# Optimization experiments

Hardware: AMD Instinct MI355X
Metric: run time of the kernel (lower is better)

## Reference

```python
import jax, jax.numpy as jnp
import numpy as np

N = 25000; E = 100000; H = 64; NODE_IN = 32; EDGE_IN = 16; L = 3


def _lin(key, fan_in, fan_out):
    kw, kb = jax.random.split(key)
    s = 1.0 / np.sqrt(fan_in)
    W = jax.random.uniform(kw, (fan_out, fan_in), minval=-s, maxval=s, dtype=jnp.float32)
    b = jax.random.uniform(kb, (fan_out,), minval=-s, maxval=s, dtype=jnp.float32)
    return W, b


def setup_inputs() -> dict:
    key = jax.random.key(0)
    ks = jax.random.split(key, 16)
    x = jax.random.normal(ks[0], (N, NODE_IN), dtype=jnp.float32)
    edge_attr = jax.random.normal(ks[1], (E, EDGE_IN), dtype=jnp.float32)
    edge_index = jax.random.randint(ks[2], (2, E), 0, N, dtype=jnp.int32)
    Wn1, bn1 = _lin(ks[3], NODE_IN, H)
    Wn2, bn2 = _lin(ks[4], H, H)
    Wn3, bn3 = _lin(ks[5], H, H)
    We1, be1 = _lin(ks[6], EDGE_IN, H)
    We2, be2 = _lin(ks[7], H, H)
    We3, be3 = _lin(ks[8], H, H * H)
    roots = jax.random.normal(ks[9], (L, H, H), dtype=jnp.float32) / np.sqrt(H)
    conv_bias = jnp.zeros((L, H), dtype=jnp.float32)
    s = 1.0 / np.sqrt(H)
    gru_Wih = jax.random.uniform(ks[10], (3 * H, H), minval=-s, maxval=s, dtype=jnp.float32)
    gru_Whh = jax.random.uniform(ks[11], (3 * H, H), minval=-s, maxval=s, dtype=jnp.float32)
    gru_bih = jax.random.uniform(ks[12], (3 * H,), minval=-s, maxval=s, dtype=jnp.float32)
    gru_bhh = jax.random.uniform(ks[13], (3 * H,), minval=-s, maxval=s, dtype=jnp.float32)
    return dict(x=x, edge_attr=edge_attr,
                Wn1=Wn1, bn1=bn1, Wn2=Wn2, bn2=bn2, Wn3=Wn3, bn3=bn3,
                We1=We1, be1=be1, We2=We2, be2=be2, We3=We3, be3=be3,
                roots=roots, conv_bias=conv_bias,
                gru_Wih=gru_Wih, gru_Whh=gru_Whh, gru_bih=gru_bih, gru_bhh=gru_bhh,
                edge_index=edge_index)


def _mpnn_forward(x, edge_attr, Wn1, bn1, Wn2, bn2, Wn3, bn3,
                  We1, be1, We2, be2, We3, be3,
                  roots, conv_bias, gru_Wih, gru_Whh, gru_bih, gru_bhh, edge_index):
    src, dst = edge_index[0], edge_index[1]
    # mlp_in: Linear-ReLU-Linear-ReLU-Linear
    h = jax.nn.relu(x @ Wn1.T + bn1)
    h = jax.nn.relu(h @ Wn2.T + bn2)
    h = h @ Wn3.T + bn3  # [N, H]
    # edge MLP is shared across all NNConv layers and edge_attr is constant -> compute once
    ew = jax.nn.relu(edge_attr @ We1.T + be1)
    ew = jax.nn.relu(ew @ We2.T + be2)
    ew = (ew @ We3.T + be3).reshape(E, H, H)  # per-edge weight [E, in, out]
    hidden = jnp.zeros((x.shape[0], H), dtype=h.dtype)  # GRU hidden (1 layer)
    for l in range(L):
        # NNConv: message_e = h[src_e] @ W_e, scatter-add to dst, plus root term and bias
        msg = jnp.einsum('ei,eio->eo', h[src], ew)
        aggr = jax.ops.segment_sum(msg, dst, num_segments=N)
        m = aggr + h @ roots[l] + conv_bias[l]  # [N, H]
        # GRU step (seq_len=1, batch=N)
        gi = m @ gru_Wih.T + gru_bih
        gh = hidden @ gru_Whh.T + gru_bhh
        i_r, i_z, i_n = jnp.split(gi, 3, axis=-1)
        h_r, h_z, h_n = jnp.split(gh, 3, axis=-1)
        r = jax.nn.sigmoid(i_r + h_r)
        z = jax.nn.sigmoid(i_z + h_z)
        n = jnp.tanh(i_n + r * h_n)
        hidden = (1.0 - z) * n + z * hidden
        h = hidden  # output of 1-layer GRU == new hidden
    return h


def reference(x, edge_attr, Wn1, bn1, Wn2, bn2, Wn3, bn3,
              We1, be1, We2, be2, We3, be3,
              roots, conv_bias, gru_Wih, gru_Whh, gru_bih, gru_bhh, edge_index):
    return _mpnn_forward(x, edge_attr, Wn1, bn1, Wn2, bn2, Wn3, bn3,
                         We1, be1, We2, be2, We3, be3,
                         roots, conv_bias, gru_Wih, gru_Whh, gru_bih, gru_bhh, edge_index)
```

## Files before the change

kernel.cpp:

```cpp
#include <hip/hip_runtime.h>
#include <math.h>

#define NN 25000
#define NE 100000

typedef _Float16 f16;
typedef _Float16 half8 __attribute__((ext_vector_type(8)));
typedef float f32x4 __attribute__((ext_vector_type(4)));

__global__ __launch_bounds__(256) void prep_all(
    const float* __restrict__ Wn1, const float* __restrict__ Wn2,
    const float* __restrict__ Wn3, const float* __restrict__ We1,
    const float* __restrict__ We2, const float* __restrict__ Wih,
    const float* __restrict__ Whh, const float* __restrict__ We3,
    const float* __restrict__ be3, float* __restrict__ T,
    f16* __restrict__ Wf16)
{
    int f = blockIdx.x * 256 + threadIdx.x;
    if (f < 39936) {
        if (f < 2048)       { int j = f;         T[f] = Wn1[(j & 63) * 32 + (j >> 6)]; }
        else if (f < 6144)  { int j = f - 2048;  T[f] = Wn2[(j & 63) * 64 + (j >> 6)]; }
        else if (f < 10240) { int j = f - 6144;  T[f] = Wn3[(j & 63) * 64 + (j >> 6)]; }
        else if (f < 11264) { int j = f - 10240; T[f] = We1[(j & 63) * 16 + (j >> 6)]; }
        else if (f < 15360) { int j = f - 11264; T[f] = We2[(j & 63) * 64 + (j >> 6)]; }
        else if (f < 27648) { int j = f - 15360; T[f] = Wih[(j % 192) * 64 + (j / 192)]; }
        else                { int j = f - 27648; T[f] = Whh[(j % 192) * 64 + (j / 192)]; }
    } else {
        int g = f - 39936;
        if (g < 262144) Wf16[g] = (f16)We3[g];
        else {
            int j = g - 262144; int o = (j >> 6), k = j & 63;
            Wf16[g] = (f16)be3[k * 64 + o];
        }
    }
}

__global__ __launch_bounds__(256) void node_mlp(
    const float* __restrict__ x, const float* __restrict__ T,
    const float* __restrict__ bn1, const float* __restrict__ bn2,
    const float* __restrict__ bn3,
    float* __restrict__ hbuf, f16* __restrict__ h16, float* __restrict__ aggr)
{
    __shared__ float sx[4][8][32];
    __shared__ float sh1[4][8][64];
    const float* Wn1T = T;
    const float* Wn2T = T + 2048;
    const float* Wn3T = T + 6144;
    int w = threadIdx.x >> 6, lane = threadIdx.x & 63;
    int n0 = blockIdx.x * 32 + w * 8;
    if (n0 >= NN) return;
    #pragma unroll
    for (int jj = 0; jj < 4; ++jj) {
        int f = jj * 64 + lane;
        sx[w][f >> 5][f & 31] = x[(size_t)(n0 + (f >> 5)) * 32 + (f & 31)];
    }
    float a[8];
    #pragma unroll
    for (int j = 0; j < 8; ++j) a[j] = bn1[lane];
    for (int i = 0; i < 32; i += 4) {
        float4 bb[8];
        #pragma unroll
        for (int j = 0; j < 8; ++j) bb[j] = *(const float4*)&sx[w][j][i];
        #pragma unroll
        for (int ii = 0; ii < 4; ++ii) {
            float wv = Wn1T[(i + ii) * 64 + lane];
            #pragma unroll
            for (int j = 0; j < 8; ++j) a[j] += ((const float*)&bb[j])[ii] * wv;
        }
    }
    #pragma unroll
    for (int j = 0; j < 8; ++j) { sh1[w][j][lane] = fmaxf(a[j], 0.f); a[j] = bn2[lane]; }
    for (int i = 0; i < 64; i += 4) {
        float4 bb[8];
        #pragma unroll
        for (int j = 0; j < 8; ++j) bb[j] = *(const float4*)&sh1[w][j][i];
        #pragma unroll
        for (int ii = 0; ii < 4; ++ii) {
            float wv = Wn2T[(i + ii) * 64 + lane];
            #pragma unroll
            for (int j = 0; j < 8; ++j) a[j] += ((const float*)&bb[j])[ii] * wv;
        }
    }
    #pragma unroll
    for (int j = 0; j < 8; ++j) { sh1[w][j][lane] = fmaxf(a[j], 0.f); a[j] = bn3[lane]; }
    for (int i = 0; i < 64; i += 4) {
        float4 bb[8];
        #pragma unroll
        for (int j = 0; j < 8; ++j) bb[j] = *(const float4*)&sh1[w][j][i];
        #pragma unroll
        for (int ii = 0; ii < 4; ++ii) {
            float wv = Wn3T[(i + ii) * 64 + lane];
            #pragma unroll
            for (int j = 0; j < 8; ++j) a[j] += ((const float*)&bb[j])[ii] * wv;
        }
    }
    #pragma unroll
    for (int j = 0; j < 8; ++j) {
        size_t idx = (size_t)(n0 + j) * 64 + lane;
        hbuf[idx] = a[j];
        h16[idx]  = (f16)a[j];
        aggr[idx] = 0.f;
    }
}

__global__ __launch_bounds__(256) void edge_mlp(
    const float* __restrict__ ea, const float* __restrict__ T,
    const float* __restrict__ be1, const float* __restrict__ be2,
    f16* __restrict__ ew16)
{
    __shared__ float sa[4][8][16];
    __shared__ float st[4][8][64];
    const float* We1T = T + 10240;
    const float* We2T = T + 11264;
    int w = threadIdx.x >> 6, lane = threadIdx.x & 63;
    int e0 = blockIdx.x * 32 + w * 8;
    if (e0 >= NE) return;
    #pragma unroll
    for (int jj = 0; jj < 2; ++jj) {
        int f = jj * 64 + lane;
        sa[w][f >> 4][f & 15] = ea[(size_t)(e0 + (f >> 4)) * 16 + (f & 15)];
    }
    float a[8];
    #pragma unroll
    for (int j = 0; j < 8; ++j) a[j] = be1[lane];
    for (int i = 0; i < 16; i += 4) {
        float4 bb[8];
        #pragma unroll
        for (int j = 0; j < 8; ++j) bb[j] = *(const float4*)&sa[w][j][i];
        #pragma unroll
        for (int ii = 0; ii < 4; ++ii) {
            float wv = We1T[(i + ii) * 64 + lane];
            #pragma unroll
            for (int j = 0; j < 8; ++j) a[j] += ((const float*)&bb[j])[ii] * wv;
        }
    }
    #pragma unroll
    for (int j = 0; j < 8; ++j) { st[w][j][lane] = fmaxf(a[j], 0.f); a[j] = be2[lane]; }
    for (int i = 0; i < 64; i += 4) {
        float4 bb[8];
        #pragma unroll
        for (int j = 0; j < 8; ++j) bb[j] = *(const float4*)&st[w][j][i];
        #pragma unroll
        for (int ii = 0; ii < 4; ++ii) {
            float wv = We2T[(i + ii) * 64 + lane];
            #pragma unroll
            for (int j = 0; j < 8; ++j) a[j] += ((const float*)&bb[j])[ii] * wv;
        }
    }
    #pragma unroll
    for (int j = 0; j < 8; ++j)
        ew16[(size_t)(e0 + j) * 64 + lane] = (f16)fmaxf(a[j], 0.f);
}

__device__ __forceinline__ half8 splat8(f16 v)
{ half8 r = { v, v, v, v, v, v, v, v }; return r; }

__device__ __forceinline__ void mfma_block(
    const char* bb, int swzA, int swzB,
    half8 aA0, half8 aA1, half8 aB0, half8 aB1, f32x4 (&acc)[2][4])
{
    half8 b00 = *(const half8*)(bb + 0    + swzA);
    half8 b01 = *(const half8*)(bb + 0    + swzB);
    half8 b10 = *(const half8*)(bb + 2048 + swzA);
    half8 b11 = *(const half8*)(bb + 2048 + swzB);
    half8 b20 = *(const half8*)(bb + 4096 + swzA);
    half8 b21 = *(const half8*)(bb + 4096 + swzB);
    half8 b30 = *(const half8*)(bb + 6144 + swzA);
    half8 b31 = *(const half8*)(bb + 6144 + swzB);
    acc[0][0] = __builtin_amdgcn_mfma_f32_16x16x32_f16(aA0, b00, acc[0][0], 0, 0, 0);
    acc[0][0] = __builtin_amdgcn_mfma_f32_16x16x32_f16(aA1, b01, acc[0][0], 0, 0, 0);
    acc[0][1] = __builtin_amdgcn_mfma_f32_16x16x32_f16(aA0, b10, acc[0][1], 0, 0, 0);
    acc[0][1] = __builtin_amdgcn_mfma_f32_16x16x32_f16(aA1, b11, acc[0][1], 0, 0, 0);
    acc[0][2] = __builtin_amdgcn_mfma_f32_16x16x32_f16(aA0, b20, acc[0][2], 0, 0, 0);
    acc[0][2] = __builtin_amdgcn_mfma_f32_16x16x32_f16(aA1, b21, acc[0][2], 0, 0, 0);
    acc[0][3] = __builtin_amdgcn_mfma_f32_16x16x32_f16(aA0, b30, acc[0][3], 0, 0, 0);
    acc[0][3] = __builtin_amdgcn_mfma_f32_16x16x32_f16(aA1, b31, acc[0][3], 0, 0, 0);
    acc[1][0] = __builtin_amdgcn_mfma_f32_16x16x32_f16(aB0, b00, acc[1][0], 0, 0, 0);
    acc[1][0] = __builtin_amdgcn_mfma_f32_16x16x32_f16(aB1, b01, acc[1][0], 0, 0, 0);
    acc[1][1] = __builtin_amdgcn_mfma_f32_16x16x32_f16(aB0, b10, acc[1][1], 0, 0, 0);
    acc[1][1] = __builtin_amdgcn_mfma_f32_16x16x32_f16(aB1, b11, acc[1][1], 0, 0, 0);
    acc[1][2] = __builtin_amdgcn_mfma_f32_16x16x32_f16(aB0, b20, acc[1][2], 0, 0, 0);
    acc[1][2] = __builtin_amdgcn_mfma_f32_16x16x32_f16(aB1, b21, acc[1][2], 0, 0, 0);
    acc[1][3] = __builtin_amdgcn_mfma_f32_16x16x32_f16(aB0, b30, acc[1][3], 0, 0, 0);
    acc[1][3] = __builtin_amdgcn_mfma_f32_16x16x32_f16(aB1, b31, acc[1][3], 0, 0, 0);
}

__global__ __launch_bounds__(256) void msg_mfma(
    const f16* __restrict__ h16, const f16* __restrict__ ew16,
    const f16* __restrict__ Wf16, const int* __restrict__ edge_index,
    float* __restrict__ aggr)
{
    __shared__ f16 sh_h[128][72];
    __shared__ f16 sh_ring[4][4096];
    __shared__ int sh_dst[128];
    int t = threadIdx.x, lane = t & 63, wv = t >> 6;
    int e0 = blockIdx.x * 128;
    char* ringc = (char*)&sh_ring[0][0];

    const uint4* gW = (const uint4*)Wf16;
    uint4 r0 = gW[t], r1 = gW[256 + t], r2 = gW[512 + t], r3 = gW[768 + t];

    {
        int row = t >> 1, part = t & 1;
        int e = e0 + row;
        bool valid = e < NE;
        int ec = valid ? e : NE - 1;
        int src = edge_index[ec];
        const uint4* hp = (const uint4*)(h16 + (size_t)src * 64 + part * 32);
        const uint4* ep = (const uint4*)(ew16 + (size_t)ec * 64 + part * 32);
        uint4 z = make_uint4(0u, 0u, 0u, 0u);
        uint4 h0 = hp[0], h1 = hp[1], h2 = hp[2], h3 = hp[3];
        uint4 g0 = valid ? ep[0] : z;
        uint4 g1 = valid ? ep[1] : z;
        uint4 g2 = valid ? ep[2] : z;
        uint4 g3 = valid ? ep[3] : z;
        *(uint4*)&sh_h[row][part * 32]      = h0;
        *(uint4*)&sh_h[row][part * 32 + 8]  = h1;
        *(uint4*)&sh_h[row][part * 32 + 16] = h2;
        *(uint4*)&sh_h[row][part * 32 + 24] = h3;
        int rb = row * 128, key = (row & 7) << 4;
        *(uint4*)(ringc + rb + ((part * 64 +  0) ^ key)) = g0;
        *(uint4*)(ringc + rb + ((part * 64 + 16) ^ key)) = g1;
        *(uint4*)(ringc + rb + ((part * 64 + 32) ^ key)) = g2;
        *(uint4*)(ringc + rb + ((part * 64 + 48) ^ key)) = g3;
        if (lane < 32) {
            int e2 = e0 + wv * 32 + lane;
            sh_dst[wv * 32 + lane] = (e2 < NE) ? edge_index[NE + e2] : -1;
        }
    }

    int r16 = lane & 15, kq = lane >> 4;
    int row0 = wv * 32 + r16, row1 = row0 + 16;

    int k0 = (row0 & 7) << 4, k1 = (row1 & 7) << 4;
    half8 evA0 = *(const half8*)(ringc + row0 * 128 + ((kq * 16) ^ k0));
    half8 evA1 = *(const half8*)(ringc + row0 * 128 + ((64 + kq * 16) ^ k0));
    half8 evB0 = *(const half8*)(ringc + row1 * 128 + ((kq * 16) ^ k1));
    half8 evB1 = *(const half8*)(ringc + row1 * 128 + ((64 + kq * 16) ^ k1));

    __syncthreads();

    int d0 = t * 16, d1 = 4096 + t * 16;
    int dsw0 = d0 ^ (((d0 >> 7) & 7) << 4);
    int dsw1 = d1 ^ (((d1 >> 7) & 7) << 4);

    *(uint4*)(ringc + dsw0) = r0;
    *(uint4*)(ringc + dsw1) = r1;
    *(uint4*)(ringc + 8192 + dsw0) = r2;
    *(uint4*)(ringc + 8192 + dsw1) = r3;
    r0 = gW[2 * 512 + t]; r1 = gW[2 * 512 + 256 + t];
    r2 = gW[3 * 512 + t]; r3 = gW[3 * 512 + 256 + t];
    __syncthreads();

    f32x4 acc[2][4];
    #pragma unroll
    for (int m = 0; m < 2; ++m)
        #pragma unroll
        for (int n = 0; n < 4; ++n) acc[m][n] = (f32x4){0, 0, 0, 0};

    int swzA = (kq << 4) ^ ((r16 & 7) << 4);
    int swzB = ((kq << 4) | 64) ^ ((r16 & 7) << 4);

    for (int i8 = 0; i8 < 8; ++i8) {
        half8 hA = *(const half8*)&sh_h[row0][i8 * 8];
        half8 hB = *(const half8*)&sh_h[row1][i8 * 8];
        #pragma unroll
        for (int w2 = 0; w2 < 4; ++w2) {
            const char* pairR = ringc + (w2 & 1) * 16384 + r16 * 128;
            #pragma unroll
            for (int s = 0; s < 2; ++s) {
                f16 hsA = hA[w2 * 2 + s];
                f16 hsB = hB[w2 * 2 + s];
                mfma_block(pairR + s * 8192, swzA, swzB,
                           evA0 * splat8(hsA), evA1 * splat8(hsA),
                           evB0 * splat8(hsB), evB1 * splat8(hsB), acc);
            }
            char* wb = ringc + ((w2 + 1) & 1) * 16384;
            *(uint4*)(wb + dsw0) = r0;
            *(uint4*)(wb + dsw1) = r1;
            *(uint4*)(wb + 8192 + dsw0) = r2;
            *(uint4*)(wb + 8192 + dsw1) = r3;
            int jw = i8 * 4 + w2;
            int sA = jw * 2 + 4; if (sA > 64) sA = 64;
            int sB = jw * 2 + 5; if (sB > 64) sB = 64;
            r0 = gW[(size_t)sA * 512 + t]; r1 = gW[(size_t)sA * 512 + 256 + t];
            r2 = gW[(size_t)sB * 512 + t]; r3 = gW[(size_t)sB * 512 + 256 + t];
            __syncthreads();
        }
    }

    {
        const char* bb = ringc + r16 * 128;
        half8 aA0 = *(const half8*)&sh_h[row0][kq * 8];
        half8 aA1 = *(const half8*)&sh_h[row0][32 + kq * 8];
        half8 aB0 = *(const half8*)&sh_h[row1][kq * 8];
        half8 aB1 = *(const half8*)&sh_h[row1][32 + kq * 8];
        mfma_block(bb, swzA, swzB, aA0, aA1, aB0, aB1, acc);
    }

    #pragma unroll
    for (int m = 0; m < 2; ++m) {
        #pragma unroll
        for (int reg = 0; reg < 4; ++reg) {
            int e_l = wv * 32 + m * 16 + kq * 4 + reg;
            int d = sh_dst[e_l];
            if (d >= 0) {
                float* ap = aggr + (size_t)d * 64 + r16;
                atomicAdd(ap,      acc[m][0][reg]);
                atomicAdd(ap + 16, acc[m][1][reg]);
                atomicAdd(ap + 32, acc[m][2][reg]);
                atomicAdd(ap + 48, acc[m][3][reg]);
            }
        }
    }
}

__global__ __launch_bounds__(256) void gru_kernel(
    float* __restrict__ aggr, float* __restrict__ hbuf, f16* __restrict__ h16,
    const float* __restrict__ root, const float* __restrict__ cbias,
    const float* __restrict__ T, const float* __restrict__ bih,
    const float* __restrict__ bhh, float* __restrict__ out2, int first)
{
    __shared__ float sm_h[4][8][64];
    __shared__ float sm_m[4][8][64];
    const float* WihT = T + 15360;
    const float* WhhT = T + 27648;
    int w = threadIdx.x >> 6, lane = threadIdx.x & 63;
    int n0 = blockIdx.x * 32 + w * 8;
    if (n0 >= NN) return;

    float hv[8], m[8];
    #pragma unroll
    for (int j = 0; j < 8; ++j) {
        size_t idx = (size_t)(n0 + j) * 64 + lane;
        hv[j] = hbuf[idx];
        sm_h[w][j][lane] = hv[j];
        m[j] = aggr[idx] + cbias[lane];
        aggr[idx] = 0.f;
    }
    for (int i = 0; i < 64; i += 4) {
        float4 bb[8];
        #pragma unroll
        for (int j = 0; j < 8; ++j) bb[j] = *(const float4*)&sm_h[w][j][i];
        #pragma unroll
        for (int ii = 0; ii < 4; ++ii) {
            float rv = root[(i + ii) * 64 + lane];
            #pragma unroll
            for (int j = 0; j < 8; ++j) m[j] += ((const float*)&bb[j])[ii] * rv;
        }
    }
    #pragma unroll
    for (int j = 0; j < 8; ++j) sm_m[w][j][lane] = m[j];

    float gr[8], gz[8], gn[8], hr[8], hz[8], hn[8];
    #pragma unroll
    for (int j = 0; j < 8; ++j) {
        gr[j] = bih[lane]; gz[j] = bih[64 + lane]; gn[j] = bih[128 + lane];
        hr[j] = bhh[lane]; hz[j] = bhh[64 + lane]; hn[j] = bhh[128 + lane];
    }
    for (int i = 0; i < 64; i += 2) {
        float2 bm[8], bh[8];
        #pragma unroll
        for (int j = 0; j < 8; ++j) {
            bm[j] = *(const float2*)&sm_m[w][j][i];
            bh[j] = *(const float2*)&sm_h[w][j][i];
        }
        #pragma unroll
        for (int ii = 0; ii < 2; ++ii) {
            float wr = WihT[(i + ii) * 192 + lane];
            float wz = WihT[(i + ii) * 192 + 64 + lane];
            float wn = WihT[(i + ii) * 192 + 128 + lane];
            #pragma unroll
            for (int j = 0; j < 8; ++j) {
                float mv = ((const float*)&bm[j])[ii];
                gr[j] += mv * wr; gz[j] += mv * wz; gn[j] += mv * wn;
            }
            if (!first) {
                float vr = WhhT[(i + ii) * 192 + lane];
                float vz = WhhT[(i + ii) * 192 + 64 + lane];
                float vn = WhhT[(i + ii) * 192 + 128 + lane];
                #pragma unroll
                for (int j = 0; j < 8; ++j) {
                    float dv = ((const float*)&bh[j])[ii];
                    hr[j] += dv * vr; hz[j] += dv * vz; hn[j] += dv * vn;
                }
            }
        }
    }

    #pragma unroll
    for (int j = 0; j < 8; ++j) {
        float r  = 1.f / (1.f + expf(-(gr[j] + hr[j])));
        float z  = 1.f / (1.f + expf(-(gz[j] + hz[j])));
        float nv = tanhf(gn[j] + r * hn[j]);
        float dvv = first ? 0.f : hv[j];
        float outv = (1.f - z) * nv + z * dvv;
        size_t idx = (size_t)(n0 + j) * 64 + lane;
        hbuf[idx] = outv;
        h16[idx]  = (f16)outv;
        if (out2) out2[idx] = outv;
    }
}

extern "C" void kernel_launch(void* const* d_in, const int* in_sizes, int n_in,
                              void* d_out, int out_size, void* d_ws, size_t ws_size,
                              hipStream_t stream)
{
    const float* x   = (const float*)d_in[0];
    const float* ea  = (const float*)d_in[1];
    const float* Wn1 = (const float*)d_in[2];  const float* bn1 = (const float*)d_in[3];
    const float* Wn2 = (const float*)d_in[4];  const float* bn2 = (const float*)d_in[5];
    const float* Wn3 = (const float*)d_in[6];  const float* bn3 = (const float*)d_in[7];
    const float* We1 = (const float*)d_in[8];  const float* be1 = (const float*)d_in[9];
    const float* We2 = (const float*)d_in[10]; const float* be2 = (const float*)d_in[11];
    const float* We3 = (const float*)d_in[12]; const float* be3 = (const float*)d_in[13];
    const float* roots = (const float*)d_in[14];
    const float* cb    = (const float*)d_in[15];
    const float* Wih = (const float*)d_in[16]; const float* Whh = (const float*)d_in[17];
    const float* bih = (const float*)d_in[18]; const float* bhh = (const float*)d_in[19];
    const int*   ei  = (const int*)d_in[20];

    float* ws   = (float*)d_ws;
    float* hbuf = ws;
    float* aggr = hbuf + (size_t)NN * 64;
    float* Tbuf = aggr + (size_t)NN * 64;
    f16*   h16  = (f16*)(ws + 2 * (size_t)NN * 64 + 40960);
    f16*   ew16 = h16  + (size_t)NN * 64;
    f16*   Wf16 = ew16 + (size_t)NE * 64;

    prep_all<<<(306176) / 256, 256, 0, stream>>>(Wn1, Wn2, Wn3, We1, We2,
                                                 Wih, Whh, We3, be3, Tbuf, Wf16);
    node_mlp<<<(NN + 31) / 32, 256, 0, stream>>>(x, Tbuf, bn1, bn2, bn3,
                                                 hbuf, h16, aggr);
    edge_mlp<<<NE / 32, 256, 0, stream>>>(ea, Tbuf, be1, be2, ew16);

    for (int l = 0; l < 3; ++l) {
        msg_mfma<<<(NE + 127) / 128, 256, 0, stream>>>(h16, ew16, Wf16, ei, aggr);
        gru_kernel<<<(NN + 31) / 32, 256, 0, stream>>>(aggr, hbuf, h16,
            roots + (size_t)l * 4096, cb + (size_t)l * 64,
            Tbuf, bih, bhh, (l == 2) ? (float*)d_out : nullptr, (l == 0) ? 1 : 0);
    }
}
```

Measured before the change: 462.9 us.

## Halve msg_mfma block to two waves with four M-tiles per wave

The message kernel now runs 128 threads (2 waves) per 128-edge block, and each wave computes four 16-row M-tiles instead of two. Each B fragment read from shared memory is reused across twice as many MFMAs, which cuts LDS traffic per MFMA. Each thread now stages twice as many weight chunks in registers, and the extra accumulators raise register pressure, which may cut occupancy even with the launch bound set to (128,2). Separately, the GRU inner loop now reads shared-memory operands as float4 instead of float2.

```diff
diff --git a/kernel.cpp b/kernel.cpp
--- a/kernel.cpp
+++ b/kernel.cpp
@@ -155,37 +155,7 @@
 __device__ __forceinline__ half8 splat8(f16 v)
 { half8 r = { v, v, v, v, v, v, v, v }; return r; }
 
-__device__ __forceinline__ void mfma_block(
-    const char* bb, int swzA, int swzB,
-    half8 aA0, half8 aA1, half8 aB0, half8 aB1, f32x4 (&acc)[2][4])
-{
-    half8 b00 = *(const half8*)(bb + 0    + swzA);
-    half8 b01 = *(const half8*)(bb + 0    + swzB);
-    half8 b10 = *(const half8*)(bb + 2048 + swzA);
-    half8 b11 = *(const half8*)(bb + 2048 + swzB);
-    half8 b20 = *(const half8*)(bb + 4096 + swzA);
-    half8 b21 = *(const half8*)(bb + 4096 + swzB);
-    half8 b30 = *(const half8*)(bb + 6144 + swzA);
-    half8 b31 = *(const half8*)(bb + 6144 + swzB);
-    acc[0][0] = __builtin_amdgcn_mfma_f32_16x16x32_f16(aA0, b00, acc[0][0], 0, 0, 0);
-    acc[0][0] = __builtin_amdgcn_mfma_f32_16x16x32_f16(aA1, b01, acc[0][0], 0, 0, 0);
-    acc[0][1] = __builtin_amdgcn_mfma_f32_16x16x32_f16(aA0, b10, acc[0][1], 0, 0, 0);
-    acc[0][1] = __builtin_amdgcn_mfma_f32_16x16x32_f16(aA1, b11, acc[0][1], 0, 0, 0);
-    acc[0][2] = __builtin_amdgcn_mfma_f32_16x16x32_f16(aA0, b20, acc[0][2], 0, 0, 0);
-    acc[0][2] = __builtin_amdgcn_mfma_f32_16x16x32_f16(aA1, b21, acc[0][2], 0, 0, 0);
-    acc[0][3] = __builtin_amdgcn_mfma_f32_16x16x32_f16(aA0, b30, acc[0][3], 0, 0, 0);
-    acc[0][3] = __builtin_amdgcn_mfma_f32_16x16x32_f16(aA1, b31, acc[0][3], 0, 0, 0);
-    acc[1][0] = __builtin_amdgcn_mfma_f32_16x16x32_f16(aB0, b00, acc[1][0], 0, 0, 0);
-    acc[1][0] = __builtin_amdgcn_mfma_f32_16x16x32_f16(aB1, b01, acc[1][0], 0, 0, 0);
-    acc[1][1] = __builtin_amdgcn_mfma_f32_16x16x32_f16(aB0, b10, acc[1][1], 0, 0, 0);
-    acc[1][1] = __builtin_amdgcn_mfma_f32_16x16x32_f16(aB1, b11, acc[1][1], 0, 0, 0);
-    acc[1][2] = __builtin_amdgcn_mfma_f32_16x16x32_f16(aB0, b20, acc[1][2], 0, 0, 0);
-    acc[1][2] = __builtin_amdgcn_mfma_f32_16x16x32_f16(aB1, b21, acc[1][2], 0, 0, 0);
-    acc[1][3] = __builtin_amdgcn_mfma_f32_16x16x32_f16(aB0, b30, acc[1][3], 0, 0, 0);
-    acc[1][3] = __builtin_amdgcn_mfma_f32_16x16x32_f16(aB1, b31, acc[1][3], 0, 0, 0);
-}
-
-__global__ __launch_bounds__(256) void msg_mfma(
+__global__ __launch_bounds__(128, 2) void msg_mfma(
     const f16* __restrict__ h16, const f16* __restrict__ ew16,
     const f16* __restrict__ Wf16, const int* __restrict__ edge_index,
     float* __restrict__ aggr)
@@ -198,63 +168,64 @@
     char* ringc = (char*)&sh_ring[0][0];
 
     const uint4* gW = (const uint4*)Wf16;
-    uint4 r0 = gW[t], r1 = gW[256 + t], r2 = gW[512 + t], r3 = gW[768 + t];
+    uint4 r[8];
+    #pragma unroll
+    for (int q = 0; q < 4; ++q) r[q]     = gW[q * 128 + t];
+    #pragma unroll
+    for (int q = 0; q < 4; ++q) r[4 + q] = gW[512 + q * 128 + t];
 
     {
-        int row = t >> 1, part = t & 1;
-        int e = e0 + row;
+        int e = e0 + t;
         bool valid = e < NE;
         int ec = valid ? e : NE - 1;
         int src = edge_index[ec];
-        const uint4* hp = (const uint4*)(h16 + (size_t)src * 64 + part * 32);
-        const uint4* ep = (const uint4*)(ew16 + (size_t)ec * 64 + part * 32);
+        const uint4* hp = (const uint4*)(h16 + (size_t)src * 64);
+        const uint4* ep = (const uint4*)(ew16 + (size_t)ec * 64);
         uint4 z = make_uint4(0u, 0u, 0u, 0u);
-        uint4 h0 = hp[0], h1 = hp[1], h2 = hp[2], h3 = hp[3];
-        uint4 g0 = valid ? ep[0] : z;
-        uint4 g1 = valid ? ep[1] : z;
-        uint4 g2 = valid ? ep[2] : z;
-        uint4 g3 = valid ? ep[3] : z;
-        *(uint4*)&sh_h[row][part * 32]      = h0;
-        *(uint4*)&sh_h[row][part * 32 + 8]  = h1;
-        *(uint4*)&sh_h[row][part * 32 + 16] = h2;
-        *(uint4*)&sh_h[row][part * 32 + 24] = h3;
-        int rb = row * 128, key = (row & 7) << 4;
-        *(uint4*)(ringc + rb + ((part * 64 +  0) ^ key)) = g0;
-        *(uint4*)(ringc + rb + ((part * 64 + 16) ^ key)) = g1;
-        *(uint4*)(ringc + rb + ((part * 64 + 32) ^ key)) = g2;
-        *(uint4*)(ringc + rb + ((part * 64 + 48) ^ key)) = g3;
-        if (lane < 32) {
-            int e2 = e0 + wv * 32 + lane;
-            sh_dst[wv * 32 + lane] = (e2 < NE) ? edge_index[NE + e2] : -1;
-        }
+        int rb = t * 128, key = (t & 7) << 4;
+        #pragma unroll
+        for (int q = 0; q < 8; ++q) {
+            uint4 hq = hp[q];
+            uint4 gq = valid ? ep[q] : z;
+            *(uint4*)&sh_h[t][q * 8] = hq;
+            *(uint4*)(ringc + rb + ((q * 16) ^ key)) = gq;
+        }
+        sh_dst[t] = valid ? edge_index[NE + e] : -1;
     }
 
     int r16 = lane & 15, kq = lane >> 4;
-    int row0 = wv * 32 + r16, row1 = row0 + 16;
-
-    int k0 = (row0 & 7) << 4, k1 = (row1 & 7) << 4;
-    half8 evA0 = *(const half8*)(ringc + row0 * 128 + ((kq * 16) ^ k0));
-    half8 evA1 = *(const half8*)(ringc + row0 * 128 + ((64 + kq * 16) ^ k0));
-    half8 evB0 = *(const half8*)(ringc + row1 * 128 + ((kq * 16) ^ k1));
-    half8 evB1 = *(const half8*)(ringc + row1 * 128 + ((64 + kq * 16) ^ k1));
+    int rowm[4];
+    #pragma unroll
+    for (int m = 0; m < 4; ++m) rowm[m] = wv * 64 + m * 16 + r16;
+
+    half8 ev0[4], ev1[4];
+    #pragma unroll
+    for (int m = 0; m < 4; ++m) {
+        int key = (rowm[m] & 7) << 4;
+        ev0[m] = *(const half8*)(ringc + rowm[m] * 128 + ((kq * 16) ^ key));
+        ev1[m] = *(const half8*)(ringc + rowm[m] * 128 + ((64 + kq * 16) ^ key));
+    }
 
     __syncthreads();
 
-    int d0 = t * 16, d1 = 4096 + t * 16;
-    int dsw0 = d0 ^ (((d0 >> 7) & 7) << 4);
-    int dsw1 = d1 ^ (((d1 >> 7) & 7) << 4);
-
-    *(uint4*)(ringc + dsw0) = r0;
-    *(uint4*)(ringc + dsw1) = r1;
-    *(uint4*)(ringc + 8192 + dsw0) = r2;
-    *(uint4*)(ringc + 8192 + dsw1) = r3;
-    r0 = gW[2 * 512 + t]; r1 = gW[2 * 512 + 256 + t];
-    r2 = gW[3 * 512 + t]; r3 = gW[3 * 512 + 256 + t];
+    int dsw[8];
+    #pragma unroll
+    for (int q = 0; q < 8; ++q) {
+        int d = q * 2048 + t * 16;
+        dsw[q] = d ^ (((d >> 7) & 7) << 4);
+    }
+
+    #pragma unroll
+    for (int q = 0; q < 8; ++q) *(uint4*)(ringc + dsw[q]) = r[q];
+    #pragma unroll
+    for (int q = 0; q < 4; ++q) r[q]     = gW[2 * 512 + q * 128 + t];
+    #pragma unroll
+    for (int q = 0; q < 4; ++q) r[4 + q] = gW[3 * 512 + q * 128 + t];
     __syncthreads();
 
-    f32x4 acc[2][4];
-    #pragma unroll
-    for (int m = 0; m < 2; ++m)
+    f32x4 acc[4][4];
+    #pragma unroll
+    for (int m = 0; m < 4; ++m)
         #pragma unroll
         for (int n = 0; n < 4; ++n) acc[m][n] = (f32x4){0, 0, 0, 0};
 
@@ -262,47 +233,82 @@
     int swzB = ((kq << 4) | 64) ^ ((r16 & 7) << 4);
 
     for (int i8 = 0; i8 < 8; ++i8) {
-        half8 hA = *(const half8*)&sh_h[row0][i8 * 8];
-        half8 hB = *(const half8*)&sh_h[row1][i8 * 8];
+        half8 hM[4];
+        #pragma unroll
+        for (int m = 0; m < 4; ++m) hM[m] = *(const half8*)&sh_h[rowm[m]][i8 * 8];
         #pragma unroll
         for (int w2 = 0; w2 < 4; ++w2) {
             const char* pairR = ringc + (w2 & 1) * 16384 + r16 * 128;
             #pragma unroll
             for (int s = 0; s < 2; ++s) {
-                f16 hsA = hA[w2 * 2 + s];
-                f16 hsB = hB[w2 * 2 + s];
-                mfma_block(pairR + s * 8192, swzA, swzB,
-                           evA0 * splat8(hsA), evA1 * splat8(hsA),
-                           evB0 * splat8(hsB), evB1 * splat8(hsB), acc);
+                const char* bb = pairR + s * 8192;
+                half8 b00 = *(const half8*)(bb + 0    + swzA);
+                half8 b01 = *(const half8*)(bb + 0    + swzB);
+                half8 b10 = *(const half8*)(bb + 2048 + swzA);
+                half8 b11 = *(const half8*)(bb + 2048 + swzB);
+                half8 b20 = *(const half8*)(bb + 4096 + swzA);
+                half8 b21 = *(const half8*)(bb + 4096 + swzB);
+                half8 b30 = *(const half8*)(bb + 6144 + swzA);
+                half8 b31 = *(const half8*)(bb + 6144 + swzB);
+                #pragma unroll
+                for (int m = 0; m < 4; ++m) {
+                    f16 hs = hM[m][w2 * 2 + s];
+                    half8 a0 = ev0[m] * splat8(hs);
+                    half8 a1 = ev1[m] * splat8(hs);
+                    acc[m][0] = __builtin_amdgcn_mfma_f32_16x16x32_f16(a0, b00, acc[m][0], 0, 0, 0);
+                    acc[m][0] = __builtin_amdgcn_mfma_f32_16x16x32_f16(a1, b01, acc[m][0], 0, 0, 0);
+                    acc[m][1] = __builtin_amdgcn_mfma_f32_16x16x32_f16(a0, b10, acc[m][1], 0, 0, 0);
+                    acc[m][1] = __builtin_amdgcn_mfma_f32_16x16x32_f16(a1, b11, acc[m][1], 0, 0, 0);
+                    acc[m][2] = __builtin_amdgcn_mfma_f32_16x16x32_f16(a0, b20, acc[m][2], 0, 0, 0);
+                    acc[m][2] = __builtin_amdgcn_mfma_f32_16x16x32_f16(a1, b21, acc[m][2], 0, 0, 0);
+                    acc[m][3] = __builtin_amdgcn_mfma_f32_16x16x32_f16(a0, b30, acc[m][3], 0, 0, 0);
+                    acc[m][3] = __builtin_amdgcn_mfma_f32_16x16x32_f16(a1, b31, acc[m][3], 0, 0, 0);
+                }
             }
             char* wb = ringc + ((w2 + 1) & 1) * 16384;
-            *(uint4*)(wb + dsw0) = r0;
-            *(uint4*)(wb + dsw1) = r1;
-            *(uint4*)(wb + 8192 + dsw0) = r2;
-            *(uint4*)(wb + 8192 + dsw1) = r3;
+            #pragma unroll
+            for (int q = 0; q < 8; ++q) *(uint4*)(wb + dsw[q]) = r[q];
             int jw = i8 * 4 + w2;
             int sA = jw * 2 + 4; if (sA > 64) sA = 64;
             int sB = jw * 2 + 5; if (sB > 64) sB = 64;
-            r0 = gW[(size_t)sA * 512 + t]; r1 = gW[(size_t)sA * 512 + 256 + t];
-            r2 = gW[(size_t)sB * 512 + t]; r3 = gW[(size_t)sB * 512 + 256 + t];
+            #pragma unroll
+            for (int q = 0; q < 4; ++q) r[q]     = gW[(size_t)sA * 512 + q * 128 + t];
+            #pragma unroll
+            for (int q = 0; q < 4; ++q) r[4 + q] = gW[(size_t)sB * 512 + q * 128 + t];
             __syncthreads();
         }
     }
 
     {
         const char* bb = ringc + r16 * 128;
-        half8 aA0 = *(const half8*)&sh_h[row0][kq * 8];
-        half8 aA1 = *(const half8*)&sh_h[row0][32 + kq * 8];
-        half8 aB0 = *(const half8*)&sh_h[row1][kq * 8];
-        half8 aB1 = *(const half8*)&sh_h[row1][32 + kq * 8];
-        mfma_block(bb, swzA, swzB, aA0, aA1, aB0, aB1, acc);
-    }
-
-    #pragma unroll
-    for (int m = 0; m < 2; ++m) {
+        half8 b00 = *(const half8*)(bb + 0    + swzA);
+        half8 b01 = *(const half8*)(bb + 0    + swzB);
+        half8 b10 = *(const half8*)(bb + 2048 + swzA);
+        half8 b11 = *(const half8*)(bb + 2048 + swzB);
+        half8 b20 = *(const half8*)(bb + 4096 + swzA);
+        half8 b21 = *(const half8*)(bb + 4096 + swzB);
+        half8 b30 = *(const half8*)(bb + 6144 + swzA);
+        half8 b31 = *(const half8*)(bb + 6144 + swzB);
+        #pragma unroll
+        for (int m = 0; m < 4; ++m) {
+            half8 a0 = *(const half8*)&sh_h[rowm[m]][kq * 8];
+            half8 a1 = *(const half8*)&sh_h[rowm[m]][32 + kq * 8];
+            acc[m][0] = __builtin_amdgcn_mfma_f32_16x16x32_f16(a0, b00, acc[m][0], 0, 0, 0);
+            acc[m][0] = __builtin_amdgcn_mfma_f32_16x16x32_f16(a1, b01, acc[m][0], 0, 0, 0);
+            acc[m][1] = __builtin_amdgcn_mfma_f32_16x16x32_f16(a0, b10, acc[m][1], 0, 0, 0);
+            acc[m][1] = __builtin_amdgcn_mfma_f32_16x16x32_f16(a1, b11, acc[m][1], 0, 0, 0);
+            acc[m][2] = __builtin_amdgcn_mfma_f32_16x16x32_f16(a0, b20, acc[m][2], 0, 0, 0);
+            acc[m][2] = __builtin_amdgcn_mfma_f32_16x16x32_f16(a1, b21, acc[m][2], 0, 0, 0);
+            acc[m][3] = __builtin_amdgcn_mfma_f32_16x16x32_f16(a0, b30, acc[m][3], 0, 0, 0);
+            acc[m][3] = __builtin_amdgcn_mfma_f32_16x16x32_f16(a1, b31, acc[m][3], 0, 0, 0);
+        }
+    }
+
+    #pragma unroll
+    for (int m = 0; m < 4; ++m) {
         #pragma unroll
         for (int reg = 0; reg < 4; ++reg) {
-            int e_l = wv * 32 + m * 16 + kq * 4 + reg;
+            int e_l = wv * 64 + m * 16 + kq * 4 + reg;
             int d = sh_dst[e_l];
             if (d >= 0) {
                 float* ap = aggr + (size_t)d * 64 + r16;
@@ -358,15 +364,15 @@
         gr[j] = bih[lane]; gz[j] = bih[64 + lane]; gn[j] = bih[128 + lane];
         hr[j] = bhh[lane]; hz[j] = bhh[64 + lane]; hn[j] = bhh[128 + lane];
     }
-    for (int i = 0; i < 64; i += 2) {
-        float2 bm[8], bh[8];
+    for (int i = 0; i < 64; i += 4) {
+        float4 bm[8], bh[8];
         #pragma unroll
         for (int j = 0; j < 8; ++j) {
-            bm[j] = *(const float2*)&sm_m[w][j][i];
-            bh[j] = *(const float2*)&sm_h[w][j][i];
-        }
-        #pragma unroll
-        for (int ii = 0; ii < 2; ++ii) {
+            bm[j] = *(const float4*)&sm_m[w][j][i];
+            bh[j] = *(const float4*)&sm_h[w][j][i];
+        }
+        #pragma unroll
+        for (int ii = 0; ii < 4; ++ii) {
             float wr = WihT[(i + ii) * 192 + lane];
             float wz = WihT[(i + ii) * 192 + 64 + lane];
             float wn = WihT[(i + ii) * 192 + 128 + lane];
@@ -435,7 +441,7 @@
     edge_mlp<<<NE / 32, 256, 0, stream>>>(ea, Tbuf, be1, be2, ew16);
 
     for (int l = 0; l < 3; ++l) {
-        msg_mfma<<<(NE + 127) / 128, 256, 0, stream>>>(h16, ew16, Wf16, ei, aggr);
+        msg_mfma<<<(NE + 127) / 128, 128, 0, stream>>>(h16, ew16, Wf16, ei, aggr);
         gru_kernel<<<(NN + 31) / 32, 256, 0, stream>>>(aggr, hbuf, h16,
             roots + (size_t)l * 4096, cb + (size_t)l * 64,
             Tbuf, bih, bhh, (l == 2) ? (float*)d_out : nullptr, (l == 0) ? 1 : 0);
```

Result: slower. 745.8 us (+61.1%).

## Move GRU and root matmuls onto fp16 MFMA with converted weights

Applied to the files above, without the earlier changes.

Replaces the scalar fp32 GRU kernel with an MFMA version that processes 64 nodes per block. Root, W_ih and W_hh are converted to fp16 in the prep kernel, and h is staged from the fp16 copy. The root term and the GRU gate products now run as 16x16x32 f16 MFMAs with fp32 accumulation. The aim is to cut the FMA-bound cost of the per-layer GRU. In exchange, the intermediate m is rounded to fp16, which loses some precision.

```diff
diff --git a/kernel.cpp b/kernel.cpp
--- a/kernel.cpp
+++ b/kernel.cpp
@@ -13,24 +13,33 @@
     const float* __restrict__ Wn3, const float* __restrict__ We1,
     const float* __restrict__ We2, const float* __restrict__ Wih,
     const float* __restrict__ Whh, const float* __restrict__ We3,
-    const float* __restrict__ be3, float* __restrict__ T,
-    f16* __restrict__ Wf16)
+    const float* __restrict__ be3, const float* __restrict__ roots,
+    float* __restrict__ T, f16* __restrict__ Wf16, f16* __restrict__ root16,
+    f16* __restrict__ Wih16, f16* __restrict__ Whh16)
 {
     int f = blockIdx.x * 256 + threadIdx.x;
-    if (f < 39936) {
+    if (f >= 318464) return;
+    if (f < 15360) {
         if (f < 2048)       { int j = f;         T[f] = Wn1[(j & 63) * 32 + (j >> 6)]; }
         else if (f < 6144)  { int j = f - 2048;  T[f] = Wn2[(j & 63) * 64 + (j >> 6)]; }
         else if (f < 10240) { int j = f - 6144;  T[f] = Wn3[(j & 63) * 64 + (j >> 6)]; }
         else if (f < 11264) { int j = f - 10240; T[f] = We1[(j & 63) * 16 + (j >> 6)]; }
-        else if (f < 15360) { int j = f - 11264; T[f] = We2[(j & 63) * 64 + (j >> 6)]; }
-        else if (f < 27648) { int j = f - 15360; T[f] = Wih[(j % 192) * 64 + (j / 192)]; }
-        else                { int j = f - 27648; T[f] = Whh[(j % 192) * 64 + (j / 192)]; }
+        else                { int j = f - 11264; T[f] = We2[(j & 63) * 64 + (j >> 6)]; }
     } else {
-        int g = f - 39936;
-        if (g < 262144) Wf16[g] = (f16)We3[g];
-        else {
-            int j = g - 262144; int o = (j >> 6), k = j & 63;
-            Wf16[g] = (f16)be3[k * 64 + o];
+        int g = f - 15360;
+        if (g < 266240) {
+            if (g < 262144) Wf16[g] = (f16)We3[g];
+            else {
+                int j = g - 262144; int o = (j >> 6), k = j & 63;
+                Wf16[g] = (f16)be3[k * 64 + o];
+            }
+        } else {
+            int g2 = g - 266240;
+            if (g2 < 12288) {
+                int l = g2 >> 12, j = g2 & 4095, o = j >> 6, i = j & 63;
+                root16[g2] = (f16)roots[l * 4096 + i * 64 + o];
+            } else if (g2 < 24576) Wih16[g2 - 12288] = (f16)Wih[g2 - 12288];
+            else                   Whh16[g2 - 24576] = (f16)Whh[g2 - 24576];
         }
     }
 }
@@ -315,90 +324,134 @@
     }
 }
 
-__global__ __launch_bounds__(256) void gru_kernel(
+__global__ __launch_bounds__(256) void gru_mfma(
     float* __restrict__ aggr, float* __restrict__ hbuf, f16* __restrict__ h16,
-    const float* __restrict__ root, const float* __restrict__ cbias,
-    const float* __restrict__ T, const float* __restrict__ bih,
-    const float* __restrict__ bhh, float* __restrict__ out2, int first)
-{
-    __shared__ float sm_h[4][8][64];
-    __shared__ float sm_m[4][8][64];
-    const float* WihT = T + 15360;
-    const float* WhhT = T + 27648;
-    int w = threadIdx.x >> 6, lane = threadIdx.x & 63;
-    int n0 = blockIdx.x * 32 + w * 8;
-    if (n0 >= NN) return;
-
-    float hv[8], m[8];
-    #pragma unroll
-    for (int j = 0; j < 8; ++j) {
-        size_t idx = (size_t)(n0 + j) * 64 + lane;
-        hv[j] = hbuf[idx];
-        sm_h[w][j][lane] = hv[j];
-        m[j] = aggr[idx] + cbias[lane];
-        aggr[idx] = 0.f;
-    }
-    for (int i = 0; i < 64; i += 4) {
-        float4 bb[8];
-        #pragma unroll
-        for (int j = 0; j < 8; ++j) bb[j] = *(const float4*)&sm_h[w][j][i];
-        #pragma unroll
-        for (int ii = 0; ii < 4; ++ii) {
-            float rv = root[(i + ii) * 64 + lane];
-            #pragma unroll
-            for (int j = 0; j < 8; ++j) m[j] += ((const float*)&bb[j])[ii] * rv;
-        }
-    }
-    #pragma unroll
-    for (int j = 0; j < 8; ++j) sm_m[w][j][lane] = m[j];
-
-    float gr[8], gz[8], gn[8], hr[8], hz[8], hn[8];
-    #pragma unroll
-    for (int j = 0; j < 8; ++j) {
-        gr[j] = bih[lane]; gz[j] = bih[64 + lane]; gn[j] = bih[128 + lane];
-        hr[j] = bhh[lane]; hz[j] = bhh[64 + lane]; hn[j] = bhh[128 + lane];
-    }
-    for (int i = 0; i < 64; i += 2) {
-        float2 bm[8], bh[8];
-        #pragma unroll
-        for (int j = 0; j < 8; ++j) {
-            bm[j] = *(const float2*)&sm_m[w][j][i];
-            bh[j] = *(const float2*)&sm_h[w][j][i];
-        }
-        #pragma unroll
-        for (int ii = 0; ii < 2; ++ii) {
-            float wr = WihT[(i + ii) * 192 + lane];
-            float wz = WihT[(i + ii) * 192 + 64 + lane];
-            float wn = WihT[(i + ii) * 192 + 128 + lane];
-            #pragma unroll
-            for (int j = 0; j < 8; ++j) {
-                float mv = ((const float*)&bm[j])[ii];
-                gr[j] += mv * wr; gz[j] += mv * wz; gn[j] += mv * wn;
+    const f16* __restrict__ root16, const float* __restrict__ cbias,
+    const f16* __restrict__ Wih16, const f16* __restrict__ Whh16,
+    const float* __restrict__ bih, const float* __restrict__ bhh,
+    float* __restrict__ out2, int first)
+{
+    __shared__ f16 sh[64][72];
+    __shared__ f16 sm[64][72];
+    int t = threadIdx.x, lane = t & 63, wv = t >> 6;
+    int n0 = blockIdx.x * 64;
+
+    {
+        int row = t >> 2, part = t & 3;
+        int n = n0 + row;
+        uint4 z = make_uint4(0u, 0u, 0u, 0u);
+        const uint4* hp = (const uint4*)(h16 + (size_t)n * 64 + part * 16);
+        uint4 v0 = (n < NN) ? hp[0] : z;
+        uint4 v1 = (n < NN) ? hp[1] : z;
+        *(uint4*)&sh[row][part * 16]     = v0;
+        *(uint4*)&sh[row][part * 16 + 8] = v1;
+    }
+    __syncthreads();
+
+    int r16 = lane & 15, kq = lane >> 4;
+    int wr = wv * 16;
+    int rowA = wr + r16;
+    half8 ah0 = *(const half8*)&sh[rowA][kq * 8];
+    half8 ah1 = *(const half8*)&sh[rowA][32 + kq * 8];
+    int nodeBase = wr + kq * 4;
+
+    f32x4 accm[4];
+    #pragma unroll
+    for (int tt = 0; tt < 4; ++tt) {
+        int o = tt * 16 + r16;
+        float cb = cbias[o];
+        #pragma unroll
+        for (int reg = 0; reg < 4; ++reg) {
+            int n = n0 + nodeBase + reg;
+            float v = 0.f;
+            if (n < NN) {
+                size_t ix = (size_t)n * 64 + o;
+                v = aggr[ix] + cb;
+                aggr[ix] = 0.f;
             }
-            if (!first) {
-                float vr = WhhT[(i + ii) * 192 + lane];
-                float vz = WhhT[(i + ii) * 192 + 64 + lane];
-                float vn = WhhT[(i + ii) * 192 + 128 + lane];
-                #pragma unroll
-                for (int j = 0; j < 8; ++j) {
-                    float dv = ((const float*)&bh[j])[ii];
-                    hr[j] += dv * vr; hz[j] += dv * vz; hn[j] += dv * vn;
-                }
-            }
-        }
-    }
-
-    #pragma unroll
-    for (int j = 0; j < 8; ++j) {
-        float r  = 1.f / (1.f + expf(-(gr[j] + hr[j])));
-        float z  = 1.f / (1.f + expf(-(gz[j] + hz[j])));
-        float nv = tanhf(gn[j] + r * hn[j]);
-        float dvv = first ? 0.f : hv[j];
-        float outv = (1.f - z) * nv + z * dvv;
-        size_t idx = (size_t)(n0 + j) * 64 + lane;
-        hbuf[idx] = outv;
-        h16[idx]  = (f16)outv;
-        if (out2) out2[idx] = outv;
+            accm[tt][reg] = v;
+        }
+    }
+    #pragma unroll
+    for (int tt = 0; tt < 4; ++tt) {
+        const f16* bp = root16 + (size_t)(tt * 16 + r16) * 64 + kq * 8;
+        half8 b0 = *(const half8*)bp;
+        half8 b1 = *(const half8*)(bp + 32);
+        accm[tt] = __builtin_amdgcn_mfma_f32_16x16x32_f16(ah0, b0, accm[tt], 0, 0, 0);
+        accm[tt] = __builtin_amdgcn_mfma_f32_16x16x32_f16(ah1, b1, accm[tt], 0, 0, 0);
+    }
+    #pragma unroll
+    for (int tt = 0; tt < 4; ++tt)
+        #pragma unroll
+        for (int reg = 0; reg < 4; ++reg)
+            sm[nodeBase + reg][tt * 16 + r16] = (f16)accm[tt][reg];
+    __syncthreads();
+    half8 am0 = *(const half8*)&sm[rowA][kq * 8];
+    half8 am1 = *(const half8*)&sm[rowA][32 + kq * 8];
+
+    f32x4 acc_rz[8], acc_in[4], acc_hn[4];
+    #pragma unroll
+    for (int tt = 0; tt < 8; ++tt) acc_rz[tt] = (f32x4){0, 0, 0, 0};
+    #pragma unroll
+    for (int tt = 0; tt < 4; ++tt) { acc_in[tt] = (f32x4){0, 0, 0, 0}; acc_hn[tt] = (f32x4){0, 0, 0, 0}; }
+
+    #pragma unroll
+    for (int tt = 0; tt < 8; ++tt) {
+        const f16* bp = Wih16 + (size_t)(tt * 16 + r16) * 64 + kq * 8;
+        half8 b0 = *(const half8*)bp;
+        half8 b1 = *(const half8*)(bp + 32);
+        acc_rz[tt] = __builtin_amdgcn_mfma_f32_16x16x32_f16(am0, b0, acc_rz[tt], 0, 0, 0);
+        acc_rz[tt] = __builtin_amdgcn_mfma_f32_16x16x32_f16(am1, b1, acc_rz[tt], 0, 0, 0);
+    }
+    #pragma unroll
+    for (int tt = 0; tt < 4; ++tt) {
+        const f16* bp = Wih16 + (size_t)(128 + tt * 16 + r16) * 64 + kq * 8;
+        half8 b0 = *(const half8*)bp;
+        half8 b1 = *(const half8*)(bp + 32);
+        acc_in[tt] = __builtin_amdgcn_mfma_f32_16x16x32_f16(am0, b0, acc_in[tt], 0, 0, 0);
+        acc_in[tt] = __builtin_amdgcn_mfma_f32_16x16x32_f16(am1, b1, acc_in[tt], 0, 0, 0);
+    }
+    if (!first) {
+        #pragma unroll
+        for (int tt = 0; tt < 8; ++tt) {
+            const f16* bp = Whh16 + (size_t)(tt * 16 + r16) * 64 + kq * 8;
+            half8 b0 = *(const half8*)bp;
+            half8 b1 = *(const half8*)(bp + 32);
+            acc_rz[tt] = __builtin_amdgcn_mfma_f32_16x16x32_f16(ah0, b0, acc_rz[tt], 0, 0, 0);
+            acc_rz[tt] = __builtin_amdgcn_mfma_f32_16x16x32_f16(ah1, b1, acc_rz[tt], 0, 0, 0);
+        }
+        #pragma unroll
+        for (int tt = 0; tt < 4; ++tt) {
+            const f16* bp = Whh16 + (size_t)(128 + tt * 16 + r16) * 64 + kq * 8;
+            half8 b0 = *(const half8*)bp;
+            half8 b1 = *(const half8*)(bp + 32);
+            acc_hn[tt] = __builtin_amdgcn_mfma_f32_16x16x32_f16(ah0, b0, acc_hn[tt], 0, 0, 0);
+            acc_hn[tt] = __builtin_amdgcn_mfma_f32_16x16x32_f16(ah1, b1, acc_hn[tt], 0, 0, 0);
+        }
+    }
+
+    #pragma unroll
+    for (int tt = 0; tt < 4; ++tt) {
+        int o = tt * 16 + r16;
+        float b_r = bih[o] + bhh[o];
+        float b_z = bih[64 + o] + bhh[64 + o];
+        float bin = bih[128 + o];
+        float bhn = bhh[128 + o];
+        #pragma unroll
+        for (int reg = 0; reg < 4; ++reg) {
+            int n = n0 + nodeBase + reg;
+            if (n >= NN) continue;
+            size_t ix = (size_t)n * 64 + o;
+            float rv = 1.f / (1.f + expf(-(acc_rz[tt][reg] + b_r)));
+            float zv = 1.f / (1.f + expf(-(acc_rz[4 + tt][reg] + b_z)));
+            float hn_ = first ? bhn : (acc_hn[tt][reg] + bhn);
+            float nv = tanhf(acc_in[tt][reg] + bin + rv * hn_);
+            float hold = first ? 0.f : hbuf[ix];
+            float outv = (1.f - zv) * nv + zv * hold;
+            hbuf[ix] = outv;
+            h16[ix]  = (f16)outv;
+            if (out2) out2[ix] = outv;
+        }
     }
 }
 
@@ -424,20 +477,24 @@
     float* hbuf = ws;
     float* aggr = hbuf + (size_t)NN * 64;
     float* Tbuf = aggr + (size_t)NN * 64;
-    f16*   h16  = (f16*)(ws + 2 * (size_t)NN * 64 + 40960);
+    f16*   h16  = (f16*)(ws + 2 * (size_t)NN * 64 + 16384);
     f16*   ew16 = h16  + (size_t)NN * 64;
     f16*   Wf16 = ew16 + (size_t)NE * 64;
-
-    prep_all<<<(306176) / 256, 256, 0, stream>>>(Wn1, Wn2, Wn3, We1, We2,
-                                                 Wih, Whh, We3, be3, Tbuf, Wf16);
+    f16*   root16 = Wf16 + 266240;
+    f16*   Wih16  = root16 + 12288;
+    f16*   Whh16  = Wih16 + 12288;
+
+    prep_all<<<(318464 + 255) / 256, 256, 0, stream>>>(Wn1, Wn2, Wn3, We1, We2,
+        Wih, Whh, We3, be3, roots, Tbuf, Wf16, root16, Wih16, Whh16);
     node_mlp<<<(NN + 31) / 32, 256, 0, stream>>>(x, Tbuf, bn1, bn2, bn3,
                                                  hbuf, h16, aggr);
     edge_mlp<<<NE / 32, 256, 0, stream>>>(ea, Tbuf, be1, be2, ew16);
 
     for (int l = 0; l < 3; ++l) {
         msg_mfma<<<(NE + 127) / 128, 256, 0, stream>>>(h16, ew16, Wf16, ei, aggr);
-        gru_kernel<<<(NN + 31) / 32, 256, 0, stream>>>(aggr, hbuf, h16,
-            roots + (size_t)l * 4096, cb + (size_t)l * 64,
-            Tbuf, bih, bhh, (l == 2) ? (float*)d_out : nullptr, (l == 0) ? 1 : 0);
-    }
-}
+        gru_mfma<<<(NN + 63) / 64, 256, 0, stream>>>(aggr, hbuf, h16,
+            root16 + (size_t)l * 4096, cb + (size_t)l * 64,
+            Wih16, Whh16, bih, bhh,
+            (l == 2) ? (float*)d_out : nullptr, (l == 0) ? 1 : 0);
+    }
+}
```

Result: faster. 409.4 us (-11.5%).
